# Optimization experiments

Hardware: AMD Instinct MI355X
Metric: run time of the kernel (lower is better)

The kernel has to match this reference:

```python
import jax, jax.numpy as jnp
import numpy as np

N_NODES = 50000
N_EDGES = 1200000
IN_DIM = 140
EDGE_DIM = 3
EMB = 64
L = 4
BN_EPS = 1e-5


def _bn(x, gamma, beta):
    # BatchNorm1d in training mode: batch statistics over axis 0 (biased var)
    mu = jnp.mean(x, axis=0)
    var = jnp.var(x, axis=0)
    return (x - mu) * jax.lax.rsqrt(var + BN_EPS) * gamma + beta


def setup_inputs() -> dict:
    key = jax.random.key(0)
    ks = jax.random.split(key, 24)
    s = lambda *sh: 0.05
    inp = {
        "x": jax.random.normal(ks[0], (N_NODES, IN_DIM), jnp.float32),
        "edge_index": jax.random.randint(ks[1], (2, N_EDGES), 0, N_NODES, jnp.int32),
        "edge_attr": jax.random.normal(ks[2], (N_EDGES, EDGE_DIM), jnp.float32),
        "lin_in_w": jax.random.normal(ks[3], (IN_DIM, EMB), jnp.float32) * 0.05,
        "lin_in_b": jnp.zeros((EMB,), jnp.float32),
        "ee_w1": jax.random.normal(ks[4], (L, EDGE_DIM, EMB), jnp.float32) * 0.1,
        "ee_b1": jnp.zeros((L, EMB), jnp.float32),
        "ee_g1": jnp.ones((L, EMB), jnp.float32),
        "ee_be1": jnp.zeros((L, EMB), jnp.float32),
        "ee_w2": jax.random.normal(ks[5], (L, EMB, EMB), jnp.float32) * 0.05,
        "ee_b2": jnp.zeros((L, EMB), jnp.float32),
        "mlp_w1": jax.random.normal(ks[6], (L, EMB, EMB), jnp.float32) * 0.05,
        "mlp_b1": jnp.zeros((L, EMB), jnp.float32),
        "mlp_g1": jnp.ones((L, EMB), jnp.float32),
        "mlp_be1": jnp.zeros((L, EMB), jnp.float32),
        "mlp_w2": jax.random.normal(ks[7], (L, EMB, EMB), jnp.float32) * 0.05,
        "mlp_b2": jnp.zeros((L, EMB), jnp.float32),
        "mlp_g2": jnp.ones((L, EMB), jnp.float32),
        "mlp_be2": jnp.zeros((L, EMB), jnp.float32),
        "lin_pred_w": jax.random.normal(ks[8], (EMB, 1), jnp.float32) * 0.05,
        "lin_pred_b": jnp.zeros((1,), jnp.float32),
    }
    return inp


def reference(x, edge_index, edge_attr, lin_in_w, lin_in_b,
              ee_w1, ee_b1, ee_g1, ee_be1, ee_w2, ee_b2,
              mlp_w1, mlp_b1, mlp_g1, mlp_be1, mlp_w2, mlp_b2, mlp_g2, mlp_be2,
              lin_pred_w, lin_pred_b):
    src, dst = edge_index[0], edge_index[1]
    n = x.shape[0]
    h = x @ lin_in_w + lin_in_b  # [N, EMB]
    for l in range(L):
        # edge encoder: Linear -> BN -> ReLU -> Linear
        e = edge_attr @ ee_w1[l] + ee_b1[l]
        e = jax.nn.relu(_bn(e, ee_g1[l], ee_be1[l]))
        e = e @ ee_w2[l] + ee_b2[l]  # [E, EMB]
        agg_e = jax.ops.segment_sum(e, dst, num_segments=n)
        hh = h + agg_e
        # GINConv (eps=0): mlp(hh + sum_{j->i} hh_j)
        msg = jax.ops.segment_sum(hh[src], dst, num_segments=n)
        z = hh + msg
        z = jax.nn.relu(_bn(z @ mlp_w1[l] + mlp_b1[l], mlp_g1[l], mlp_be1[l]))
        z = jax.nn.relu(_bn(z @ mlp_w2[l] + mlp_b2[l], mlp_g2[l], mlp_be2[l]))
        h = h + z  # residual in GINModel.forward
    out = h @ lin_pred_w + lin_pred_b
    return out[:, 0]
```

## Files before the change

kernel.cpp:

```cpp
#include <hip/hip_runtime.h>

#define EMB 64
#define INDIM 140
#define NL 4
#define EPS 1e-5f

__device__ __forceinline__ float bnrelu(float v, float sum, float sq, float g, float be, float invN){
  float mu  = sum*invN;
  float var = fmaf(-mu, mu, sq*invN);
  float sc  = g * rsqrtf(var + EPS);
  return fmaxf(fmaf(v - mu, sc, be), 0.f);
}

__global__ __launch_bounds__(256) void k_pass1(const int* __restrict__ dst,
    const float* __restrict__ ea, int E, int* __restrict__ deg, float* __restrict__ est)
{
  __shared__ float ls[9];
  if (threadIdx.x < 9) ls[threadIdx.x] = 0.f;
  __syncthreads();
  int tid = blockIdx.x*blockDim.x + threadIdx.x;
  int stride = gridDim.x*blockDim.x;
  float a0=0,a1=0,a2=0,p00=0,p11=0,p22=0,p01=0,p02=0,p12=0;
  for (int e=tid;e<E;e+=stride){
    atomicAdd(&deg[dst[e]],1);
    float d0=ea[3*e+0], d1=ea[3*e+1], d2=ea[3*e+2];
    a0+=d0;a1+=d1;a2+=d2;
    p00=fmaf(d0,d0,p00); p11=fmaf(d1,d1,p11); p22=fmaf(d2,d2,p22);
    p01=fmaf(d0,d1,p01); p02=fmaf(d0,d2,p02); p12=fmaf(d1,d2,p12);
  }
  #pragma unroll
  for (int off=32; off>0; off>>=1){
    a0+=__shfl_down(a0,off); a1+=__shfl_down(a1,off); a2+=__shfl_down(a2,off);
    p00+=__shfl_down(p00,off); p11+=__shfl_down(p11,off); p22+=__shfl_down(p22,off);
    p01+=__shfl_down(p01,off); p02+=__shfl_down(p02,off); p12+=__shfl_down(p12,off);
  }
  if ((threadIdx.x & 63)==0){
    atomicAdd(&ls[0],a0); atomicAdd(&ls[1],a1); atomicAdd(&ls[2],a2);
    atomicAdd(&ls[3],p00); atomicAdd(&ls[4],p11); atomicAdd(&ls[5],p22);
    atomicAdd(&ls[6],p01); atomicAdd(&ls[7],p02); atomicAdd(&ls[8],p12);
  }
  __syncthreads();
  if (threadIdx.x < 9) atomicAdd(&est[threadIdx.x*16], ls[threadIdx.x]);
}

__global__ __launch_bounds__(256) void k_scanA(const int* __restrict__ deg,
    int* __restrict__ bsum, int n)
{
  int b = blockIdx.x, t = threadIdx.x;
  int i0 = b*1024 + t*4;
  int s = 0;
  if (i0+3 < n){ int4 v = *(const int4*)(deg+i0); s = v.x+v.y+v.z+v.w; }
  else { for (int j=0;j<4;j++){ int i=i0+j; if (i<n) s += deg[i]; } }
  #pragma unroll
  for (int off=32;off>0;off>>=1) s += __shfl_down(s, off);
  __shared__ int ws[4];
  if ((t&63)==0) ws[t>>6] = s;
  __syncthreads();
  if (t==0) bsum[b] = ws[0]+ws[1]+ws[2]+ws[3];
}

__global__ __launch_bounds__(64) void k_scanB(const int* __restrict__ bsum,
    int* __restrict__ boff, int* __restrict__ rs, int nb, int n)
{
  int t = threadIdx.x;
  int carry = 0;
  for (int base=0; base<nb; base+=64){
    int idx = base + t;
    int v = (idx<nb)? bsum[idx] : 0;
    int x = v;
    #pragma unroll
    for (int off=1;off<64;off<<=1){ int u = __shfl_up(x, off); if (t>=off) x += u; }
    if (idx<nb) boff[idx] = carry + x - v;
    int tot = __shfl(x, 63);
    carry += tot;
  }
  if (t==0) rs[n] = carry;
}

__global__ __launch_bounds__(256) void k_scanC(int* __restrict__ deg,
    const int* __restrict__ boff, int* __restrict__ rs, int n)
{
  int b = blockIdx.x, t = threadIdx.x;
  int i0 = b*1024 + t*4;
  int a=0,c=0,d=0,e=0;
  if (i0+3 < n){ int4 v = *(const int4*)(deg+i0); a=v.x;c=v.y;d=v.z;e=v.w; }
  else { if(i0<n)a=deg[i0]; if(i0+1<n)c=deg[i0+1]; if(i0+2<n)d=deg[i0+2]; if(i0+3<n)e=deg[i0+3]; }
  int s4 = a+c+d+e;
  int x = s4;
  int lane = t & 63;
  #pragma unroll
  for (int off=1;off<64;off<<=1){ int u = __shfl_up(x, off); if (lane>=off) x += u; }
  int wexcl = x - s4;
  __shared__ int ws[4];
  if (lane==63) ws[t>>6] = x;
  __syncthreads();
  int base = boff[b];
  int wid = t>>6;
  for (int j=0;j<wid;j++) base += ws[j];
  int p = base + wexcl;
  int r0=p, r1=p+a, r2=p+a+c, r3=p+a+c+d;
  if (i0+3 < n){
    *(int4*)(rs+i0)  = make_int4(r0,r1,r2,r3);
    *(int4*)(deg+i0) = make_int4(r0,r1,r2,r3);
  } else {
    if(i0<n){rs[i0]=r0;deg[i0]=r0;} if(i0+1<n){rs[i0+1]=r1;deg[i0+1]=r1;}
    if(i0+2<n){rs[i0+2]=r2;deg[i0+2]=r2;} if(i0+3<n){rs[i0+3]=r3;deg[i0+3]=r3;}
  }
}

__global__ __launch_bounds__(256) void k_scatter(const int* __restrict__ src,
    const int* __restrict__ dst, const float* __restrict__ ea, int E,
    int* __restrict__ cur, float4* __restrict__ rec)
{
  int tid = blockIdx.x*blockDim.x + threadIdx.x;
  int stride = gridDim.x*blockDim.x;
  for (int e=tid;e<E;e+=stride){
    int d = dst[e];
    int p = atomicAdd(&cur[d], 1);
    rec[p] = make_float4(ea[3*e+0], ea[3*e+1], ea[3*e+2], (float)src[e]);
  }
}

__global__ __launch_bounds__(256) void k_prec(const float* __restrict__ est,
  const float* __restrict__ w1, const float* __restrict__ b1,
  const float* __restrict__ g1, const float* __restrict__ be1,
  float* __restrict__ ac, float invE)
{
  int t = threadIdx.x; int l = t>>6, c = t&63;
  float m0 = est[0]*invE, m1 = est[16]*invE, m2 = est[32]*invE;
  float c00 = est[48]*invE - m0*m0, c11 = est[64]*invE - m1*m1, c22 = est[80]*invE - m2*m2;
  float c01 = est[96]*invE - m0*m1, c02 = est[112]*invE - m0*m2, c12 = est[128]*invE - m1*m2;
  float w0 = w1[(l*3+0)*64+c], w1_ = w1[(l*3+1)*64+c], w2_ = w1[(l*3+2)*64+c];
  float b = b1[l*64+c], g = g1[l*64+c], be = be1[l*64+c];
  float mu = m0*w0 + m1*w1_ + m2*w2_ + b;
  float var = w0*w0*c00 + w1_*w1_*c11 + w2_*w2_*c22
            + 2.f*(w0*w1_*c01 + w0*w2_*c02 + w1_*w2_*c12);
  float sc = g * rsqrtf(var + EPS);
  float* o = ac + l*256 + c*4;
  o[0] = w0*sc; o[1] = w1_*sc; o[2] = w2_*sc; o[3] = (b - mu)*sc + be;
}

__global__ __launch_bounds__(256) void k_h0(const float* __restrict__ x,
  const float* __restrict__ w, const float* __restrict__ b, float* __restrict__ h, int n)
{
  __shared__ float4 s_x[4][280];
  int wv = (blockIdx.x*256 + threadIdx.x) >> 6;
  int wslot = (threadIdx.x >> 6) & 3;
  int lane = threadIdx.x & 63;
  int i0 = wv*8;
  int m = n - i0; if (m > 8) m = 8; if (m < 0) m = 0;
  int limit = m*35;
  const float4* xp4 = (const float4*)(x + (size_t)i0*INDIM);
  #pragma unroll
  for (int j=0;j<5;j++){
    int idx = j*64 + lane;
    if (idx < limit) s_x[wslot][idx] = xp4[idx];
  }
  __syncthreads();
  float acc[8];
  float bl = b[lane];
  #pragma unroll
  for (int t=0;t<8;t++) acc[t] = bl;
  const float* wcol = w + lane;
  #pragma unroll 1
  for (int kq=0; kq<35; kq++){
    float w0 = wcol[(4*kq+0)*EMB];
    float w1 = wcol[(4*kq+1)*EMB];
    float w2 = wcol[(4*kq+2)*EMB];
    float w3 = wcol[(4*kq+3)*EMB];
    #pragma unroll
    for (int t=0;t<8;t++){
      float4 xv = s_x[wslot][t*35 + kq];
      acc[t] = fmaf(xv.x, w0, acc[t]);
      acc[t] = fmaf(xv.y, w1, acc[t]);
      acc[t] = fmaf(xv.z, w2, acc[t]);
      acc[t] = fmaf(xv.w, w3, acc[t]);
    }
  }
  #pragma unroll
  for (int t=0;t<8;t++)
    if (t < m) h[(size_t)(i0+t)*EMB + lane] = acc[t];
}

__global__ __launch_bounds__(256) void k_l1(
  float* __restrict__ h, float* __restrict__ hh, const float* __restrict__ yprev,
  const int* __restrict__ rs, const float4* __restrict__ rec,
  const float* __restrict__ ac, const float* __restrict__ w2, const float* __restrict__ b2,
  const float* __restrict__ st2, const float* __restrict__ g2, const float* __restrict__ be2,
  int n, int update, float invN)
{
  __shared__ float4 ldsr[4][4][16];
  int wv = (blockIdx.x*256 + threadIdx.x) >> 6;
  int wslot = (threadIdx.x >> 6) & 3;
  int lane = threadIdx.x & 63;
  int i0 = wv*4;
  float4 a = ((const float4*)ac)[lane];
  float b2l = b2[lane];
  float accv[4];
  #pragma unroll
  for (int t=0;t<4;t++){
    int i = i0 + t;
    bool act = (i < n);
    int ii = act ? i : 0;
    int e0 = rs[ii], e1 = rs[ii+1];
    float racc = 0.f;
    int e = e0;
    for (; e+4<=e1; e+=4){
      float4 d0 = rec[e], d1 = rec[e+1], d2 = rec[e+2], d3 = rec[e+3];
      racc += fmaxf(fmaf(d0.x,a.x,fmaf(d0.y,a.y,fmaf(d0.z,a.z,a.w))),0.f);
      racc += fmaxf(fmaf(d1.x,a.x,fmaf(d1.y,a.y,fmaf(d1.z,a.z,a.w))),0.f);
      racc += fmaxf(fmaf(d2.x,a.x,fmaf(d2.y,a.y,fmaf(d2.z,a.z,a.w))),0.f);
      racc += fmaxf(fmaf(d3.x,a.x,fmaf(d3.y,a.y,fmaf(d3.z,a.z,a.w))),0.f);
    }
    for (; e<e1; e++){
      float4 d0 = rec[e];
      racc += fmaxf(fmaf(d0.x,a.x,fmaf(d0.y,a.y,fmaf(d0.z,a.z,a.w))),0.f);
    }
    ((float*)&ldsr[wslot][t])[lane] = racc;
    float hv = h[(size_t)ii*EMB + lane];
    if (update){
      float yv = yprev[(size_t)ii*EMB + lane];
      hv += bnrelu(yv, st2[lane*16], st2[(64+lane)*16], g2[lane], be2[lane], invN);
      if (act) h[(size_t)i*EMB + lane] = hv;
    }
    float degf = (float)(e1 - e0);
    accv[t] = fmaf(degf, b2l, hv);
  }
  __syncthreads();
  const float* wcol = w2 + lane;
  #pragma unroll 1
  for (int kq=0; kq<16; kq++){
    float w0 = wcol[(4*kq+0)*EMB];
    float w1v = wcol[(4*kq+1)*EMB];
    float w2v = wcol[(4*kq+2)*EMB];
    float w3 = wcol[(4*kq+3)*EMB];
    #pragma unroll
    for (int t=0;t<4;t++){
      float4 rv = ldsr[wslot][t][kq];
      accv[t] = fmaf(rv.x, w0, accv[t]);
      accv[t] = fmaf(rv.y, w1v, accv[t]);
      accv[t] = fmaf(rv.z, w2v, accv[t]);
      accv[t] = fmaf(rv.w, w3, accv[t]);
    }
  }
  #pragma unroll
  for (int t=0;t<4;t++)
    if (i0+t < n) hh[(size_t)(i0+t)*EMB + lane] = accv[t];
}

__global__ __launch_bounds__(256) void k_l2(
  const float* __restrict__ hh, const int* __restrict__ rs, const float* __restrict__ recw,
  const float* __restrict__ w1, const float* __restrict__ b1,
  float* __restrict__ y, int n)
{
  __shared__ float4 ldsz[4][4][16];
  int wv = (blockIdx.x*256 + threadIdx.x) >> 6;
  int wslot = (threadIdx.x >> 6) & 3;
  int lane = threadIdx.x & 63;
  int i0 = wv*4;
  #pragma unroll
  for (int t=0;t<4;t++){
    int i = i0 + t;
    bool act = (i < n);
    int ii = act ? i : 0;
    int e0 = rs[ii], e1 = rs[ii+1];
    float zc = hh[(size_t)ii*EMB + lane];
    int e = e0;
    for (; e+4<=e1; e+=4){
      int s0 = (int)recw[4*e+3];
      int s1 = (int)recw[4*e+7];
      int s2 = (int)recw[4*e+11];
      int s3 = (int)recw[4*e+15];
      zc += hh[(size_t)s0*EMB + lane];
      zc += hh[(size_t)s1*EMB + lane];
      zc += hh[(size_t)s2*EMB + lane];
      zc += hh[(size_t)s3*EMB + lane];
    }
    for (; e<e1; e++){
      int s0 = (int)recw[4*e+3];
      zc += hh[(size_t)s0*EMB + lane];
    }
    ((float*)&ldsz[wslot][t])[lane] = zc;
  }
  __syncthreads();
  float b1l = b1[lane];
  float accv[4];
  #pragma unroll
  for (int t=0;t<4;t++) accv[t] = b1l;
  const float* wcol = w1 + lane;
  #pragma unroll 1
  for (int kq=0; kq<16; kq++){
    float w0 = wcol[(4*kq+0)*EMB];
    float w1v = wcol[(4*kq+1)*EMB];
    float w2v = wcol[(4*kq+2)*EMB];
    float w3 = wcol[(4*kq+3)*EMB];
    #pragma unroll
    for (int t=0;t<4;t++){
      float4 zv = ldsz[wslot][t][kq];
      accv[t] = fmaf(zv.x, w0, accv[t]);
      accv[t] = fmaf(zv.y, w1v, accv[t]);
      accv[t] = fmaf(zv.z, w2v, accv[t]);
      accv[t] = fmaf(zv.w, w3, accv[t]);
    }
  }
  #pragma unroll
  for (int t=0;t<4;t++)
    if (i0+t < n) y[(size_t)(i0+t)*EMB + lane] = accv[t];
}

__global__ __launch_bounds__(256) void k_l3(float* __restrict__ y,
  const float* __restrict__ st1, const float* __restrict__ g1, const float* __restrict__ be1,
  const float* __restrict__ w2, const float* __restrict__ b2, int n, float invN)
{
  __shared__ float4 ldst[4][4][16];
  int wv = (blockIdx.x*256 + threadIdx.x) >> 6;
  int wslot = (threadIdx.x >> 6) & 3;
  int lane = threadIdx.x & 63;
  int i0 = wv*4;
  float s1 = st1[lane*16], sq1 = st1[(64+lane)*16];
  float g1l = g1[lane], be1l = be1[lane];
  #pragma unroll
  for (int t=0;t<4;t++){
    int i = i0 + t;
    int ii = (i < n) ? i : 0;
    float yv = y[(size_t)ii*EMB + lane];
    ((float*)&ldst[wslot][t])[lane] = bnrelu(yv, s1, sq1, g1l, be1l, invN);
  }
  __syncthreads();
  float b2l = b2[lane];
  float accv[4];
  #pragma unroll
  for (int t=0;t<4;t++) accv[t] = b2l;
  const float* wcol = w2 + lane;
  #pragma unroll 1
  for (int kq=0; kq<16; kq++){
    float w0 = wcol[(4*kq+0)*EMB];
    float w1v = wcol[(4*kq+1)*EMB];
    float w2v = wcol[(4*kq+2)*EMB];
    float w3 = wcol[(4*kq+3)*EMB];
    #pragma unroll
    for (int t=0;t<4;t++){
      float4 tv = ldst[wslot][t][kq];
      accv[t] = fmaf(tv.x, w0, accv[t]);
      accv[t] = fmaf(tv.y, w1v, accv[t]);
      accv[t] = fmaf(tv.z, w2v, accv[t]);
      accv[t] = fmaf(tv.w, w3, accv[t]);
    }
  }
  #pragma unroll
  for (int t=0;t<4;t++)
    if (i0+t < n) y[(size_t)(i0+t)*EMB + lane] = accv[t];
}

__global__ __launch_bounds__(256) void k_stats(const float* __restrict__ y,
    float* __restrict__ st, int n)
{
  __shared__ float ls[128];
  int lane = threadIdx.x & 63;
  int wid  = threadIdx.x >> 6;
  int gw = blockIdx.x*4 + wid;
  int nw = gridDim.x*4;
  float s=0.f, q=0.f;
  for (int i=gw; i<n; i+=nw){
    float v = y[(size_t)i*EMB + lane];
    s += v; q = fmaf(v,v,q);
  }
  if (threadIdx.x < 128) ls[threadIdx.x] = 0.f;
  __syncthreads();
  atomicAdd(&ls[lane], s); atomicAdd(&ls[64+lane], q);
  __syncthreads();
  if (threadIdx.x < 128) atomicAdd(&st[threadIdx.x*16], ls[threadIdx.x]);
}

__global__ __launch_bounds__(64) void k_out(
  const float* __restrict__ h, const float* __restrict__ y,
  const float* __restrict__ st2, const float* __restrict__ g2, const float* __restrict__ be2,
  const float* __restrict__ wp, const float* __restrict__ bp,
  float* __restrict__ out, int n, float invN)
{
  int i = blockIdx.x*64 + threadIdx.x; if (i>=n) return;
  const float* hr = h + (size_t)i*EMB;
  const float* yr = y + (size_t)i*EMB;
  float acc = 0.f;
  #pragma unroll
  for (int q=0;q<16;q++){
    int c0=q*4;
    float4 hv = *(const float4*)(hr+c0);
    float4 yv = *(const float4*)(yr+c0);
    float f0 = hv.x + bnrelu(yv.x, st2[(c0+0)*16], st2[(64+c0+0)*16], g2[c0+0], be2[c0+0], invN);
    float f1 = hv.y + bnrelu(yv.y, st2[(c0+1)*16], st2[(64+c0+1)*16], g2[c0+1], be2[c0+1], invN);
    float f2 = hv.z + bnrelu(yv.z, st2[(c0+2)*16], st2[(64+c0+2)*16], g2[c0+2], be2[c0+2], invN);
    float f3 = hv.w + bnrelu(yv.w, st2[(c0+3)*16], st2[(64+c0+3)*16], g2[c0+3], be2[c0+3], invN);
    acc = fmaf(f0, wp[c0+0], acc);
    acc = fmaf(f1, wp[c0+1], acc);
    acc = fmaf(f2, wp[c0+2], acc);
    acc = fmaf(f3, wp[c0+3], acc);
  }
  out[i] = acc + bp[0];
}

extern "C" void kernel_launch(void* const* d_in, const int* in_sizes, int n_in,
                              void* d_out, int out_size, void* d_ws, size_t ws_size,
                              hipStream_t stream)
{
  const float* x        = (const float*)d_in[0];
  const int*   ei       = (const int*)d_in[1];
  const float* ea       = (const float*)d_in[2];
  const float* lin_in_w = (const float*)d_in[3];
  const float* lin_in_b = (const float*)d_in[4];
  const float* ee_w1    = (const float*)d_in[5];
  const float* ee_b1    = (const float*)d_in[6];
  const float* ee_g1    = (const float*)d_in[7];
  const float* ee_be1   = (const float*)d_in[8];
  const float* ee_w2    = (const float*)d_in[9];
  const float* ee_b2    = (const float*)d_in[10];
  const float* mlp_w1   = (const float*)d_in[11];
  const float* mlp_b1   = (const float*)d_in[12];
  const float* mlp_g1   = (const float*)d_in[13];
  const float* mlp_be1  = (const float*)d_in[14];
  const float* mlp_w2   = (const float*)d_in[15];
  const float* mlp_b2   = (const float*)d_in[16];
  const float* mlp_g2   = (const float*)d_in[17];
  const float* mlp_be2  = (const float*)d_in[18];
  const float* pred_w   = (const float*)d_in[19];
  const float* pred_b   = (const float*)d_in[20];

  int n = in_sizes[0] / INDIM;
  int E = in_sizes[1] / 2;
  const int* srcp = ei;
  const int* dstp = ei + E;

  char* w = (char*)d_ws;
  auto al = [](size_t o){ return (o + 255) & ~(size_t)255; };
  size_t o = 0;
  int*   deg = (int*)(w + o);  o += (size_t)n*4;  o = al(o);
  float* est = (float*)(w + o); o += 144*4;  o = al(o);
  float* nst = (float*)(w + o); o += (size_t)NL*2*2048*4;
  size_t zero_bytes = o;
  o = al(o); int* rs   = (int*)(w + o);   o += (size_t)(n+1)*4;
  o = al(o); int* bsum = (int*)(w + o);   o += 256*4;
  o = al(o); int* boff = (int*)(w + o);   o += 256*4;
  o = al(o); float4* rec = (float4*)(w + o); o += (size_t)E*16;
  o = al(o); float* acb = (float*)(w + o); o += (size_t)NL*256*4;
  o = al(o); float* h   = (float*)(w + o); o += (size_t)n*EMB*4;
  o = al(o); float* hhb = (float*)(w + o); o += (size_t)n*EMB*4;
  o = al(o); float* yb  = (float*)(w + o); o += (size_t)n*EMB*4;

  (void)hipMemsetAsync(d_ws, 0, zero_bytes, stream);

  int nbChunk = (n + 1023)/1024;
  k_pass1<<<512, 256, 0, stream>>>(dstp, ea, E, deg, est);
  k_scanA<<<nbChunk, 256, 0, stream>>>(deg, bsum, n);
  k_scanB<<<1, 64, 0, stream>>>(bsum, boff, rs, nbChunk, n);
  k_scanC<<<nbChunk, 256, 0, stream>>>(deg, boff, rs, n);
  k_scatter<<<1024, 256, 0, stream>>>(srcp, dstp, ea, E, deg , rec);
  k_prec<<<1, 256, 0, stream>>>(est, ee_w1, ee_b1, ee_g1, ee_be1, acb, 1.f/(float)E);

  int nb_h0 = ((n + 7)/8 + 3)/4;
  int nb_l  = (n + 15)/16;
  float invN = 1.f/(float)n;
  k_h0<<<nb_h0, 256, 0, stream>>>(x, lin_in_w, lin_in_b, h, n);

  for (int l=0; l<NL; l++){
    float* st1 = nst + (size_t)l*4096;
    float* st2 = st1 + 2048;
    const float* st2prev = (l>0) ? (nst + (size_t)(l-1)*4096 + 2048) : nst;
    const float* g2p  = (l>0) ? (mlp_g2  + (size_t)(l-1)*64) : mlp_g2;
    const float* be2p = (l>0) ? (mlp_be2 + (size_t)(l-1)*64) : mlp_be2;
    k_l1<<<nb_l, 256, 0, stream>>>(h, hhb, yb, rs, rec,
        acb + (size_t)l*256, ee_w2 + (size_t)l*4096, ee_b2 + (size_t)l*64,
        st2prev, g2p, be2p, n, (l>0)?1:0, invN);
    k_l2<<<nb_l, 256, 0, stream>>>(hhb, rs, (const float*)rec,
        mlp_w1 + (size_t)l*4096, mlp_b1 + (size_t)l*64, yb, n);
    k_stats<<<256, 256, 0, stream>>>(yb, st1, n);
    k_l3<<<nb_l, 256, 0, stream>>>(yb, st1,
        mlp_g1 + (size_t)l*64, mlp_be1 + (size_t)l*64,
        mlp_w2 + (size_t)l*4096, mlp_b2 + (size_t)l*64, n, invN);
    k_stats<<<256, 256, 0, stream>>>(yb, st2, n);
  }
  k_out<<<(n+63)/64, 64, 0, stream>>>(h, yb,
      nst + (size_t)(NL-1)*4096 + 2048, mlp_g2 + (size_t)(NL-1)*64, mlp_be2 + (size_t)(NL-1)*64,
      pred_w, pred_b, (float*)d_out, n, invN);
}
```

Baseline: 1.001 ms.

## Fuse BN statistics into matmul kernels with per-block partials and deterministic reduce

Result: faster. 961.4 us (-3.9%).

```diff
diff --git a/kernel.cpp b/kernel.cpp
--- a/kernel.cpp
+++ b/kernel.cpp
@@ -205,12 +205,17 @@
     int e0 = rs[ii], e1 = rs[ii+1];
     float racc = 0.f;
     int e = e0;
-    for (; e+4<=e1; e+=4){
-      float4 d0 = rec[e], d1 = rec[e+1], d2 = rec[e+2], d3 = rec[e+3];
+    for (; e+8<=e1; e+=8){
+      float4 d0 = rec[e],   d1 = rec[e+1], d2 = rec[e+2], d3 = rec[e+3];
+      float4 d4 = rec[e+4], d5 = rec[e+5], d6 = rec[e+6], d7 = rec[e+7];
       racc += fmaxf(fmaf(d0.x,a.x,fmaf(d0.y,a.y,fmaf(d0.z,a.z,a.w))),0.f);
       racc += fmaxf(fmaf(d1.x,a.x,fmaf(d1.y,a.y,fmaf(d1.z,a.z,a.w))),0.f);
       racc += fmaxf(fmaf(d2.x,a.x,fmaf(d2.y,a.y,fmaf(d2.z,a.z,a.w))),0.f);
       racc += fmaxf(fmaf(d3.x,a.x,fmaf(d3.y,a.y,fmaf(d3.z,a.z,a.w))),0.f);
+      racc += fmaxf(fmaf(d4.x,a.x,fmaf(d4.y,a.y,fmaf(d4.z,a.z,a.w))),0.f);
+      racc += fmaxf(fmaf(d5.x,a.x,fmaf(d5.y,a.y,fmaf(d5.z,a.z,a.w))),0.f);
+      racc += fmaxf(fmaf(d6.x,a.x,fmaf(d6.y,a.y,fmaf(d6.z,a.z,a.w))),0.f);
+      racc += fmaxf(fmaf(d7.x,a.x,fmaf(d7.y,a.y,fmaf(d7.z,a.z,a.w))),0.f);
     }
     for (; e<e1; e++){
       float4 d0 = rec[e];
@@ -251,13 +256,15 @@
 __global__ __launch_bounds__(256) void k_l2(
   const float* __restrict__ hh, const int* __restrict__ rs, const float* __restrict__ recw,
   const float* __restrict__ w1, const float* __restrict__ b1,
-  float* __restrict__ y, int n)
+  float* __restrict__ y, float* __restrict__ pst, int n)
 {
   __shared__ float4 ldsz[4][4][16];
+  __shared__ float ls[128];
   int wv = (blockIdx.x*256 + threadIdx.x) >> 6;
   int wslot = (threadIdx.x >> 6) & 3;
   int lane = threadIdx.x & 63;
   int i0 = wv*4;
+  if (threadIdx.x < 128) ls[threadIdx.x] = 0.f;
   #pragma unroll
   for (int t=0;t<4;t++){
     int i = i0 + t;
@@ -266,15 +273,24 @@
     int e0 = rs[ii], e1 = rs[ii+1];
     float zc = hh[(size_t)ii*EMB + lane];
     int e = e0;
-    for (; e+4<=e1; e+=4){
-      int s0 = (int)recw[4*e+3];
-      int s1 = (int)recw[4*e+7];
-      int s2 = (int)recw[4*e+11];
-      int s3 = (int)recw[4*e+15];
-      zc += hh[(size_t)s0*EMB + lane];
-      zc += hh[(size_t)s1*EMB + lane];
-      zc += hh[(size_t)s2*EMB + lane];
-      zc += hh[(size_t)s3*EMB + lane];
+    for (; e+8<=e1; e+=8){
+      int s0 = (int)recw[4*(e+0)+3];
+      int s1 = (int)recw[4*(e+1)+3];
+      int s2 = (int)recw[4*(e+2)+3];
+      int s3 = (int)recw[4*(e+3)+3];
+      int s4 = (int)recw[4*(e+4)+3];
+      int s5 = (int)recw[4*(e+5)+3];
+      int s6 = (int)recw[4*(e+6)+3];
+      int s7 = (int)recw[4*(e+7)+3];
+      float g0 = hh[(size_t)s0*EMB + lane];
+      float g1 = hh[(size_t)s1*EMB + lane];
+      float g2 = hh[(size_t)s2*EMB + lane];
+      float g3 = hh[(size_t)s3*EMB + lane];
+      float g4 = hh[(size_t)s4*EMB + lane];
+      float g5 = hh[(size_t)s5*EMB + lane];
+      float g6 = hh[(size_t)s6*EMB + lane];
+      float g7 = hh[(size_t)s7*EMB + lane];
+      zc += ((g0+g1)+(g2+g3)) + ((g4+g5)+(g6+g7));
     }
     for (; e<e1; e++){
       int s0 = (int)recw[4*e+3];
@@ -303,20 +319,32 @@
       accv[t] = fmaf(zv.w, w3, accv[t]);
     }
   }
-  #pragma unroll
-  for (int t=0;t<4;t++)
-    if (i0+t < n) y[(size_t)(i0+t)*EMB + lane] = accv[t];
+  float ssum = 0.f, ssq = 0.f;
+  #pragma unroll
+  for (int t=0;t<4;t++){
+    if (i0+t < n){
+      y[(size_t)(i0+t)*EMB + lane] = accv[t];
+      ssum += accv[t];
+      ssq = fmaf(accv[t], accv[t], ssq);
+    }
+  }
+  atomicAdd(&ls[lane], ssum); atomicAdd(&ls[64+lane], ssq);
+  __syncthreads();
+  if (threadIdx.x < 128) pst[(size_t)blockIdx.x*128 + threadIdx.x] = ls[threadIdx.x];
 }
 
 __global__ __launch_bounds__(256) void k_l3(float* __restrict__ y,
   const float* __restrict__ st1, const float* __restrict__ g1, const float* __restrict__ be1,
-  const float* __restrict__ w2, const float* __restrict__ b2, int n, float invN)
+  const float* __restrict__ w2, const float* __restrict__ b2,
+  float* __restrict__ pst, int n, float invN)
 {
   __shared__ float4 ldst[4][4][16];
+  __shared__ float ls[128];
   int wv = (blockIdx.x*256 + threadIdx.x) >> 6;
   int wslot = (threadIdx.x >> 6) & 3;
   int lane = threadIdx.x & 63;
   int i0 = wv*4;
+  if (threadIdx.x < 128) ls[threadIdx.x] = 0.f;
   float s1 = st1[lane*16], sq1 = st1[(64+lane)*16];
   float g1l = g1[lane], be1l = be1[lane];
   #pragma unroll
@@ -347,29 +375,32 @@
       accv[t] = fmaf(tv.w, w3, accv[t]);
     }
   }
-  #pragma unroll
-  for (int t=0;t<4;t++)
-    if (i0+t < n) y[(size_t)(i0+t)*EMB + lane] = accv[t];
-}
-
-__global__ __launch_bounds__(256) void k_stats(const float* __restrict__ y,
-    float* __restrict__ st, int n)
-{
-  __shared__ float ls[128];
-  int lane = threadIdx.x & 63;
-  int wid  = threadIdx.x >> 6;
-  int gw = blockIdx.x*4 + wid;
-  int nw = gridDim.x*4;
-  float s=0.f, q=0.f;
-  for (int i=gw; i<n; i+=nw){
-    float v = y[(size_t)i*EMB + lane];
-    s += v; q = fmaf(v,v,q);
-  }
-  if (threadIdx.x < 128) ls[threadIdx.x] = 0.f;
-  __syncthreads();
-  atomicAdd(&ls[lane], s); atomicAdd(&ls[64+lane], q);
-  __syncthreads();
-  if (threadIdx.x < 128) atomicAdd(&st[threadIdx.x*16], ls[threadIdx.x]);
+  float ssum = 0.f, ssq = 0.f;
+  #pragma unroll
+  for (int t=0;t<4;t++){
+    if (i0+t < n){
+      y[(size_t)(i0+t)*EMB + lane] = accv[t];
+      ssum += accv[t];
+      ssq = fmaf(accv[t], accv[t], ssq);
+    }
+  }
+  atomicAdd(&ls[lane], ssum); atomicAdd(&ls[64+lane], ssq);
+  __syncthreads();
+  if (threadIdx.x < 128) pst[(size_t)blockIdx.x*128 + threadIdx.x] = ls[threadIdx.x];
+}
+
+__global__ __launch_bounds__(256) void k_red(const float* __restrict__ pst,
+    float* __restrict__ st, int nb)
+{
+  int ch = blockIdx.x;
+  float s = 0.f;
+  for (int i=threadIdx.x; i<nb; i+=256) s += pst[(size_t)i*128 + ch];
+  #pragma unroll
+  for (int off=32; off>0; off>>=1) s += __shfl_down(s, off);
+  __shared__ float ws[4];
+  if ((threadIdx.x&63)==0) ws[threadIdx.x>>6] = s;
+  __syncthreads();
+  if (threadIdx.x==0) st[ch*16] = ws[0]+ws[1]+ws[2]+ws[3];
 }
 
 __global__ __launch_bounds__(64) void k_out(
@@ -435,8 +466,8 @@
   size_t o = 0;
   int*   deg = (int*)(w + o);  o += (size_t)n*4;  o = al(o);
   float* est = (float*)(w + o); o += 144*4;  o = al(o);
-  float* nst = (float*)(w + o); o += (size_t)NL*2*2048*4;
   size_t zero_bytes = o;
+  o = al(o); float* nst = (float*)(w + o); o += (size_t)NL*2*2048*4;
   o = al(o); int* rs   = (int*)(w + o);   o += (size_t)(n+1)*4;
   o = al(o); int* bsum = (int*)(w + o);   o += 256*4;
   o = al(o); int* boff = (int*)(w + o);   o += 256*4;
@@ -445,6 +476,7 @@
   o = al(o); float* h   = (float*)(w + o); o += (size_t)n*EMB*4;
   o = al(o); float* hhb = (float*)(w + o); o += (size_t)n*EMB*4;
   o = al(o); float* yb  = (float*)(w + o); o += (size_t)n*EMB*4;
+  o = al(o); float* pst = (float*)(w + o); o += (size_t)4096*128*4;
 
   (void)hipMemsetAsync(d_ws, 0, zero_bytes, stream);
 
@@ -471,12 +503,12 @@
         acb + (size_t)l*256, ee_w2 + (size_t)l*4096, ee_b2 + (size_t)l*64,
         st2prev, g2p, be2p, n, (l>0)?1:0, invN);
     k_l2<<<nb_l, 256, 0, stream>>>(hhb, rs, (const float*)rec,
-        mlp_w1 + (size_t)l*4096, mlp_b1 + (size_t)l*64, yb, n);
-    k_stats<<<256, 256, 0, stream>>>(yb, st1, n);
+        mlp_w1 + (size_t)l*4096, mlp_b1 + (size_t)l*64, yb, pst, n);
+    k_red<<<128, 256, 0, stream>>>(pst, st1, nb_l);
     k_l3<<<nb_l, 256, 0, stream>>>(yb, st1,
         mlp_g1 + (size_t)l*64, mlp_be1 + (size_t)l*64,
-        mlp_w2 + (size_t)l*4096, mlp_b2 + (size_t)l*64, n, invN);
-    k_stats<<<256, 256, 0, stream>>>(yb, st2, n);
+        mlp_w2 + (size_t)l*4096, mlp_b2 + (size_t)l*64, pst, n, invN);
+    k_red<<<128, 256, 0, stream>>>(pst, st2, nb_l);
   }
   k_out<<<(n+63)/64, 64, 0, stream>>>(h, yb,
       nst + (size_t)(NL-1)*4096 + 2048, mlp_g2 + (size_t)(NL-1)*64, mlp_be2 + (size_t)(NL-1)*64,
```
